# Optimization experiments

Measured on AMD Instinct MI355X. Metric: run time of the kernel, lower is better.

The kernel has to match this reference:

```python
import jax, jax.numpy as jnp
import numpy as np

B, S, HID, NH = 2, 2048, 1024, 16
HD = HID // NH
SCALE = HD ** -0.5


def elu_plus_one(x):
    return jax.nn.elu(x) + 1.0


def setup_inputs() -> dict:
    key = jax.random.key(0)
    ks = jax.random.split(key, 8)
    w_scale = 0.02  # keep logits in a sane range
    return {
        "hidden_states": jax.random.normal(ks[0], (B, S, HID), jnp.float32),
        "wq": jax.random.normal(ks[1], (HID, HID), jnp.float32) * w_scale,
        "wk": jax.random.normal(ks[2], (HID, HID), jnp.float32) * w_scale,
        "wv": jax.random.normal(ks[3], (HID, HID), jnp.float32) * w_scale,
        "wo": jax.random.normal(ks[4], (HID, HID), jnp.float32) * w_scale,
        "beta": jax.random.normal(ks[5], (NH,), jnp.float32),
        "memory": jax.random.normal(ks[6], (NH, HD, HD), jnp.float32),
        "memory_norm": jax.random.uniform(ks[7], (NH, HD), jnp.float32),
    }


def reference(hidden_states, wq, wk, wv, wo, beta, memory, memory_norm):
    b, s, _ = hidden_states.shape
    # nn.Linear(bias=False): x @ W^T; weights stored [out, in]
    def proj(x, w):
        return jnp.einsum("bsh,oh->bso", x, w).reshape(b, s, NH, HD).transpose(0, 2, 1, 3)

    q = proj(hidden_states, wq)  # [B,H,S,D]
    k = proj(hidden_states, wk)
    v = proj(hidden_states, wv)

    # local causal softmax attention (materializes [B,H,S,S] as the original does)
    scores = jnp.einsum("bhsd,bhtd->bhst", q, k) * SCALE
    causal_mask = jnp.triu(jnp.full((s, s), -jnp.inf, dtype=scores.dtype), k=1)
    attn = jax.nn.softmax(scores + causal_mask, axis=-1)
    a_local = jnp.einsum("bhst,bhtd->bhsd", attn, v)

    # compressive memory retrieval: sigma(Q) @ M / (sigma(Q) @ z)
    sigma_q = elu_plus_one(q)
    a_mem_unnorm = jnp.einsum("bhsd,hde->bhse", sigma_q, memory)
    norm = jnp.clip(jnp.einsum("bhsd,hd->bhs", sigma_q, memory_norm), 1e-6, None)
    a_mem = a_mem_unnorm / norm[..., None]

    gate = jax.nn.sigmoid(beta).reshape(1, NH, 1, 1)
    combined = gate * a_mem + (1.0 - gate) * a_local  # [B,H,S,D]
    combined = combined.transpose(0, 2, 1, 3).reshape(b, s, HID)
    return jnp.einsum("bsh,oh->bso", combined, wo)
```

## Files before the change

kernel.cpp:

```cpp
#include <hip/hip_runtime.h>
#include <stdint.h>

#define LOG2E 1.4426950408889634f

typedef __attribute__((ext_vector_type(8))) __bf16 bf16x8;
typedef __attribute__((ext_vector_type(4))) __bf16 bf16x4;
typedef __attribute__((ext_vector_type(4))) float f32x4;

__device__ inline void gll16(const void* g, void* l) {
  __builtin_amdgcn_global_load_lds(
      (const __attribute__((address_space(1))) void*)g,
      (__attribute__((address_space(3))) void*)l, 16, 0, 0);
}

__global__ __launch_bounds__(256) void cvt_all(
    const float* __restrict__ hs, const float* __restrict__ wq,
    const float* __restrict__ wk, const float* __restrict__ wv,
    const float* __restrict__ wo,
    __bf16* __restrict__ hsb, __bf16* __restrict__ wqb, __bf16* __restrict__ wkb,
    __bf16* __restrict__ wvb, __bf16* __restrict__ wob) {
  int bid = blockIdx.x;
  const float* s; __bf16* d; int i;
  if (bid < 4096) { s = hs; d = hsb; i = bid * 256 + threadIdx.x; }
  else {
    int seg = (bid - 4096) >> 10;
    i = ((bid - 4096) & 1023) * 256 + threadIdx.x;
    s = seg == 0 ? wq : seg == 1 ? wk : seg == 2 ? wv : wo;
    d = seg == 0 ? wqb : seg == 1 ? wkb : seg == 2 ? wvb : wob;
  }
  float4 v = ((const float4*)s)[i];
  bf16x4 o;
  o[0] = (__bf16)v.x; o[1] = (__bf16)v.y; o[2] = (__bf16)v.z; o[3] = (__bf16)v.w;
  *(bf16x4*)&d[(size_t)i * 4] = o;
}

#define KSCALE 0.18033688011112042f
__global__ __launch_bounds__(256, 3) void qkv_gemm(
    const __bf16* __restrict__ hsb, const __bf16* __restrict__ wqb,
    const __bf16* __restrict__ wkb, const __bf16* __restrict__ wvb,
    __bf16* __restrict__ qbuf, __bf16* __restrict__ kbuf,
    __bf16* __restrict__ vtb) {
  constexpr int K = 1024;
  __shared__ __align__(16) __bf16 lta[128 * 32];
  __shared__ __align__(16) __bf16 ltb[128 * 32];
  const int bid = blockIdx.x;
  const int z = bid >> 8, r = bid & 255;
  const __bf16 *A, *Bt;
  int m0, n0;
  if (z < 2) {
    A = hsb; Bt = z ? wkb : wqb;
    m0 = (r & 31) * 128; n0 = (r >> 5) * 128;
  } else {
    A = wvb; Bt = hsb;
    m0 = (r & 7) * 128; n0 = (r >> 3) * 128;
  }
  const int tid = threadIdx.x;
  const int w = tid >> 6, l = tid & 63;
  const int lg = l >> 4, lr = l & 15;
  const int wm = (w >> 1) * 64, wn = (w & 1) * 64;
  f32x4 acc[4][4] = {};
  const int srow = w * 16 + (l >> 2);
  const int scol = (l & 3) * 8;
  const __bf16* ga = A + (size_t)(m0 + srow) * K + scol;
  const __bf16* gb = Bt + (size_t)(n0 + srow) * K + scol;
  __bf16* la = &lta[(size_t)w * 16 * 32];
  __bf16* lb = &ltb[(size_t)w * 16 * 32];
  for (int k0 = 0; k0 < K; k0 += 32) {
    __syncthreads();
    gll16(ga + k0, la);
    gll16(ga + 64 * K + k0, la + 64 * 32);
    gll16(gb + k0, lb);
    gll16(gb + 64 * K + k0, lb + 64 * 32);
    __syncthreads();
    bf16x8 af[4], bfr[4];
#pragma unroll
    for (int i = 0; i < 4; ++i) {
      af[i]  = *(const bf16x8*)&lta[(wm + i * 16 + lr) * 32 + lg * 8];
      bfr[i] = *(const bf16x8*)&ltb[(wn + i * 16 + lr) * 32 + lg * 8];
    }
#pragma unroll
    for (int i = 0; i < 4; ++i)
#pragma unroll
      for (int j = 0; j < 4; ++j)
        acc[i][j] = __builtin_amdgcn_mfma_f32_16x16x32_bf16(af[i], bfr[j], acc[i][j], 0, 0, 0);
  }
#pragma unroll
  for (int i = 0; i < 4; ++i)
#pragma unroll
    for (int j = 0; j < 4; ++j)
#pragma unroll
      for (int rr = 0; rr < 4; ++rr) {
        int gm = m0 + wm + i * 16 + lg * 4 + rr;
        int gn = n0 + wn + j * 16 + lr;
        float v = acc[i][j][rr];
        if (z < 2) {
          int bb = gm >> 11, s = gm & 2047, hh = gn >> 6, d = gn & 63;
          __bf16* dst = z ? kbuf : qbuf;
          if (z) v *= KSCALE;
          dst[(((size_t)bb * 16 + hh) * 2048 + s) * 64 + d] = (__bf16)v;
        } else {
          int bb = gn >> 11, s = gn & 2047, hh = gm >> 6, d = gm & 63;
          vtb[(((size_t)bb * 16 + hh) * 64 + d) * 2048 + s] = (__bf16)v;
        }
      }
}

__global__ __launch_bounds__(256, 2) void gemm_out(const __bf16* __restrict__ A,
                                                   const __bf16* __restrict__ Bt,
                                                   float* __restrict__ C,
                                                   int M, int N) {
  constexpr int K = 1024;
  __shared__ __align__(16) __bf16 lta[128 * 32];
  __shared__ __align__(16) __bf16 ltb[64 * 32];
  const int tid = threadIdx.x;
  const int w = tid >> 6, l = tid & 63;
  const int lg = l >> 4, lr = l & 15;
  const int m0 = blockIdx.x * 128, n0 = blockIdx.y * 64;
  const int wm = (w >> 1) * 64, wn = (w & 1) * 32;
  f32x4 acc[4][2] = {};
  const int srow = tid >> 2;
  const int scol = (tid & 3) * 8;
  const __bf16* ga = A + (size_t)(m0 + srow) * K + scol;
  const __bf16* gb = Bt + (size_t)(n0 + srow) * K + scol;
  __bf16* la = &lta[(size_t)w * 512];
  __bf16* lb = &ltb[(size_t)w * 512];
  for (int k0 = 0; k0 < K; k0 += 32) {
    __syncthreads();
    gll16(ga + k0, la);
    gll16(ga + (size_t)64 * K + k0, la + 64 * 32);
    gll16(gb + k0, lb);
    __syncthreads();
    bf16x8 af[4], bfr[2];
#pragma unroll
    for (int i = 0; i < 4; ++i)
      af[i]  = *(const bf16x8*)&lta[(wm + i * 16 + lr) * 32 + lg * 8];
#pragma unroll
    for (int j = 0; j < 2; ++j)
      bfr[j] = *(const bf16x8*)&ltb[(wn + j * 16 + lr) * 32 + lg * 8];
#pragma unroll
    for (int i = 0; i < 4; ++i)
#pragma unroll
      for (int j = 0; j < 2; ++j)
        acc[i][j] = __builtin_amdgcn_mfma_f32_16x16x32_bf16(af[i], bfr[j], acc[i][j], 0, 0, 0);
  }
#pragma unroll
  for (int i = 0; i < 4; ++i)
#pragma unroll
    for (int j = 0; j < 2; ++j)
#pragma unroll
      for (int rr = 0; rr < 4; ++rr) {
        int gm = m0 + wm + i * 16 + lg * 4 + rr;
        int gn = n0 + wn + j * 16 + lr;
        C[(size_t)gm * N + gn] = acc[i][j][rr];
      }
}

#define DEFER_THR 11.5f
#define SWZ(row, col) (((row) << 7) + ((col) ^ (((row) & 7) << 3)))
#define SWZK(row, col) (((row) << 6) + ((col) ^ (((row) & 7) << 3)))

__global__ __launch_bounds__(256, 5) void attn_kernel(
    const __bf16* __restrict__ qb,
    const __bf16* __restrict__ kb,
    const __bf16* __restrict__ vtb,
    const float* __restrict__ memory,
    const float* __restrict__ memnorm,
    const float* __restrict__ beta,
    __bf16* __restrict__ comb)
{
  __shared__ __align__(16) __bf16 kt[128 * 64];
  __shared__ __align__(16) __bf16 vt[64 * 128];

  const int tid = threadIdx.x;
  const int w = tid >> 6, l = tid & 63;
  const int lg = l >> 4, lr = l & 15;
  const int t = 31 - (blockIdx.x >> 5);
  const int bh = blockIdx.x & 31;
  const int hh = bh & 15, b = bh >> 4;
  const int wq0 = t * 64 + w * 16;
  const int ntiles = (t >> 1) + 1;

  const int k_row = tid >> 3;
  const int k_col = ((tid & 7) ^ (k_row & 7)) * 8;
  const __bf16* ksrc = kb + ((size_t)bh * 2048 + k_row) * 64 + k_col;
  const int v_d = tid >> 4;
  const int v_col = ((tid & 15) ^ (v_d & 7)) * 8;
  const __bf16* vsrc = vtb + ((size_t)bh * 64 + v_d) * 2048 + v_col;
  __bf16* kdst = &kt[w * 512];
  __bf16* vdst = &vt[w * 512];

  bf16x8 qf[2];
#pragma unroll
  for (int kk = 0; kk < 2; ++kk)
    qf[kk] = *(const bf16x8*)(qb + ((size_t)bh * 2048 + wq0 + lr) * 64 + kk * 32 + lg * 8);

  float mrun = -1e30f, lsum = 0.f;
  f32x4 apv[4] = {};

  for (int kv = 0; kv < ntiles; ++kv) {
    const int kv0 = kv * 128;
    __syncthreads();
#pragma unroll
    for (int i = 0; i < 4; ++i) {
      gll16(ksrc + (size_t)(kv0 + i * 32) * 64, kdst + i * 2048);
      gll16(vsrc + (size_t)i * 16 * 2048 + kv0, vdst + i * 2048);
    }
    __syncthreads();

    f32x4 sc[8] = {};
#pragma unroll
    for (int kk = 0; kk < 2; ++kk)
#pragma unroll
      for (int nf = 0; nf < 8; ++nf) {
        bf16x8 kf = *(const bf16x8*)&kt[SWZK(nf * 16 + lr, kk * 32 + lg * 8)];
        sc[nf] = __builtin_amdgcn_mfma_f32_16x16x32_bf16(kf, qf[kk], sc[nf], 0, 0, 0);
      }

    const int qrow = wq0 + lr;
    if (kv == ntiles - 1) {
#pragma unroll
      for (int nf = 0; nf < 8; ++nf)
#pragma unroll
        for (int r = 0; r < 4; ++r)
          if (kv0 + nf * 16 + lg * 4 + r > qrow) sc[nf][r] = -1e30f;
    }

    f32x4 m4 = sc[0];
#pragma unroll
    for (int nf = 1; nf < 8; ++nf)
#pragma unroll
      for (int r = 0; r < 4; ++r) m4[r] = fmaxf(m4[r], sc[nf][r]);
    float mx = fmaxf(fmaxf(m4[0], m4[1]), fmaxf(m4[2], m4[3]));
    mx = fmaxf(mx, __shfl_xor(mx, 16, 64));
    mx = fmaxf(mx, __shfl_xor(mx, 32, 64));

    if (!__all(mx - mrun <= DEFER_THR)) {
      float mold = mrun;
      float mn = fmaxf(mold, mx);
      mrun = mn;
      float scl = __builtin_amdgcn_exp2f(mold - mn);
      lsum *= scl;
      float sclq[4];
#pragma unroll
      for (int r = 0; r < 4; ++r) sclq[r] = __shfl(scl, (lg << 2) | r, 16);
#pragma unroll
      for (int nf = 0; nf < 4; ++nf)
#pragma unroll
        for (int r = 0; r < 4; ++r) apv[nf][r] *= sclq[r];
    }

    f32x4 rs4 = {0.f, 0.f, 0.f, 0.f};
#pragma unroll
    for (int nf = 0; nf < 8; ++nf)
#pragma unroll
      for (int r = 0; r < 4; ++r) {
        float pv = __builtin_amdgcn_exp2f(sc[nf][r] - mrun);
        sc[nf][r] = pv;
        rs4[r] += pv;
      }
    float rs = (rs4[0] + rs4[1]) + (rs4[2] + rs4[3]);
    rs += __shfl_xor(rs, 16, 64);
    rs += __shfl_xor(rs, 32, 64);
    lsum += rs;

#pragma unroll
    for (int kk = 0; kk < 4; ++kk) {
      uint32_t a0, a1, b0, b1;
      asm("v_cvt_pk_bf16_f32 %0, %1, %2" : "=v"(a0) : "v"(sc[2 * kk][0]), "v"(sc[2 * kk][1]));
      asm("v_cvt_pk_bf16_f32 %0, %1, %2" : "=v"(a1) : "v"(sc[2 * kk][2]), "v"(sc[2 * kk][3]));
      asm("v_cvt_pk_bf16_f32 %0, %1, %2" : "=v"(b0) : "v"(sc[2 * kk + 1][0]), "v"(sc[2 * kk + 1][1]));
      asm("v_cvt_pk_bf16_f32 %0, %1, %2" : "=v"(b1) : "v"(sc[2 * kk + 1][2]), "v"(sc[2 * kk + 1][3]));
      asm("v_permlane32_swap_b32 %0, %1" : "+v"(a0), "+v"(b0));
      asm("v_permlane32_swap_b32 %0, %1" : "+v"(a1), "+v"(b1));
      asm("v_permlane16_swap_b32 %0, %1" : "+v"(a0), "+v"(b0));
      asm("v_permlane16_swap_b32 %0, %1" : "+v"(a1), "+v"(b1));
      union { uint32_t u[4]; bf16x8 v; } pa;
      pa.u[0] = a0;
      pa.u[1] = a1;
      pa.u[2] = b0;
      pa.u[3] = b1;
#pragma unroll
      for (int nf = 0; nf < 4; ++nf) {
        bf16x8 vf = *(const bf16x8*)&vt[SWZ(nf * 16 + lr, kk * 32 + lg * 8)];
        apv[nf] = __builtin_amdgcn_mfma_f32_16x16x32_bf16(pa.v, vf, apv[nf], 0, 0, 0);
      }
    }
  }

  __syncthreads();
  __bf16* mt = kt;
  for (int i = tid; i < 64 * 64; i += 256) {
    int d = i >> 6, e = i & 63;
    mt[e * 72 + d] = (__bf16)memory[((size_t)hh * 64 + d) * 64 + e];
  }
  for (int i = tid; i < 16 * 64; i += 256) {
    int e = 64 + (i >> 6), d = i & 63;
    mt[e * 72 + d] = (__bf16)memnorm[hh * 64 + d];
  }
  __syncthreads();

  bf16x8 sf[2];
#pragma unroll
  for (int kk = 0; kk < 2; ++kk) {
    bf16x8 q = qf[kk], s;
#pragma unroll
    for (int j = 0; j < 8; ++j) {
      float x = (float)q[j];
      float sg = x > 0.f ? x + 1.f : __builtin_amdgcn_exp2f(x * LOG2E);
      s[j] = (__bf16)sg;
    }
    sf[kk] = s;
  }

  f32x4 am[5] = {};
#pragma unroll
  for (int kk = 0; kk < 2; ++kk)
#pragma unroll
    for (int nf = 0; nf < 5; ++nf) {
      bf16x8 bb = *(const bf16x8*)&mt[(nf * 16 + lr) * 72 + kk * 32 + lg * 8];
      am[nf] = __builtin_amdgcn_mfma_f32_16x16x32_bf16(sf[kk], bb, am[nf], 0, 0, 0);
    }

  const float gate = 1.f / (1.f + __builtin_amdgcn_exp2f(-beta[hh] * LOG2E));
  const float og = 1.f - gate;
  float lsq[4];
#pragma unroll
  for (int r = 0; r < 4; ++r) lsq[r] = __shfl(lsum, (lg << 2) | r, 16);
#pragma unroll
  for (int r = 0; r < 4; ++r) {
    int row = wq0 + lg * 4 + r;
    float linv = __builtin_amdgcn_rcpf(lsq[r]);
    float nrm = fmaxf(am[4][r], 1e-6f);
    float ninv = __builtin_amdgcn_rcpf(nrm);
    size_t base = ((size_t)b * 2048 + row) * 1024 + hh * 64;
#pragma unroll
    for (int nf = 0; nf < 4; ++nf) {
      float al = apv[nf][r] * linv;
      float amv = am[nf][r] * ninv;
      comb[base + nf * 16 + lr] = (__bf16)(gate * amv + og * al);
    }
  }
}

extern "C" void kernel_launch(void* const* d_in, const int* in_sizes, int n_in,
                              void* d_out, int out_size, void* d_ws, size_t ws_size,
                              hipStream_t stream) {
  const float* hs      = (const float*)d_in[0];
  const float* wq      = (const float*)d_in[1];
  const float* wk      = (const float*)d_in[2];
  const float* wv      = (const float*)d_in[3];
  const float* wo      = (const float*)d_in[4];
  const float* beta    = (const float*)d_in[5];
  const float* memory  = (const float*)d_in[6];
  const float* memnorm = (const float*)d_in[7];
  float* out = (float*)d_out;

  char* ws = (char*)d_ws;
  __bf16* hsb  = (__bf16*)(ws);
  __bf16* wqb  = (__bf16*)(ws + ((size_t)8  << 20));
  __bf16* wkb  = (__bf16*)(ws + ((size_t)10 << 20));
  __bf16* wvb  = (__bf16*)(ws + ((size_t)12 << 20));
  __bf16* wob  = (__bf16*)(ws + ((size_t)14 << 20));
  __bf16* qbuf = (__bf16*)(ws + ((size_t)16 << 20));
  __bf16* kbuf = (__bf16*)(ws + ((size_t)24 << 20));
  __bf16* vtb  = (__bf16*)(ws + ((size_t)32 << 20));
  __bf16* comb = (__bf16*)(ws + ((size_t)40 << 20));

  cvt_all<<<8192, 256, 0, stream>>>(hs, wq, wk, wv, wo, hsb, wqb, wkb, wvb, wob);

  qkv_gemm<<<768, 256, 0, stream>>>(hsb, wqb, wkb, wvb, qbuf, kbuf, vtb);

  attn_kernel<<<1024, 256, 0, stream>>>(qbuf, kbuf, vtb, memory, memnorm, beta, comb);

  gemm_out<<<dim3(32, 16), 256, 0, stream>>>(comb, wob, out, 4096, 1024);
}
```

Measured before the change: 104.3 us.

## Split KV range for long causal query tiles and merge partials in separate kernel

The 16 heaviest query-tile rows of the causal attention are each split into two blocks that process halves of the KV range. Each half writes its unnormalized output in bf16 along with its running max and sum. A new merge kernel combines the two halves, computes the memory retrieval and the gate, and writes the combined output. The aim is to even out the load across blocks in the triangular workload. The cost is an extra kernel launch, partial-result traffic through the workspace, and bf16 rounding of the partial outputs. The partials reuse the hsb workspace region, which is safe only because hsb is no longer needed after the QKV GEMM.

```diff
diff --git a/kernel.cpp b/kernel.cpp
--- a/kernel.cpp
+++ b/kernel.cpp
@@ -166,7 +166,9 @@
     const float* __restrict__ memory,
     const float* __restrict__ memnorm,
     const float* __restrict__ beta,
-    __bf16* __restrict__ comb)
+    __bf16* __restrict__ comb,
+    __bf16* __restrict__ pOb,
+    float* __restrict__ pML)
 {
   __shared__ __align__(16) __bf16 kt[128 * 64];
   __shared__ __align__(16) __bf16 vt[64 * 128];
@@ -174,11 +176,17 @@
   const int tid = threadIdx.x;
   const int w = tid >> 6, l = tid & 63;
   const int lg = l >> 4, lr = l & 15;
-  const int t = 31 - (blockIdx.x >> 5);
+  const int idx = blockIdx.x >> 5;
   const int bh = blockIdx.x & 31;
   const int hh = bh & 15, b = bh >> 4;
+  const bool split = idx < 32;
+  const int t = split ? (31 - (idx >> 1)) : (47 - idx);
+  const int half = split ? (idx & 1) : 0;
   const int wq0 = t * 64 + w * 16;
-  const int ntiles = (t >> 1) + 1;
+  const int ntt = (t >> 1) + 1;
+  const int cA = (ntt + 1) >> 1;
+  const int kvb = (split && half) ? cA : 0;
+  const int nloc = split ? (half ? ntt - cA : cA) : ntt;
 
   const int k_row = tid >> 3;
   const int k_col = ((tid & 7) ^ (k_row & 7)) * 8;
@@ -197,8 +205,9 @@
   float mrun = -1e30f, lsum = 0.f;
   f32x4 apv[4] = {};
 
-  for (int kv = 0; kv < ntiles; ++kv) {
-    const int kv0 = kv * 128;
+  for (int kv = 0; kv < nloc; ++kv) {
+    const int kvg = kvb + kv;
+    const int kv0 = kvg * 128;
     __syncthreads();
 #pragma unroll
     for (int i = 0; i < 4; ++i) {
@@ -217,7 +226,7 @@
       }
 
     const int qrow = wq0 + lr;
-    if (kv == ntiles - 1) {
+    if (kvg == ntt - 1) {
 #pragma unroll
       for (int nf = 0; nf < 8; ++nf)
 #pragma unroll
@@ -275,16 +284,27 @@
       asm("v_permlane16_swap_b32 %0, %1" : "+v"(a0), "+v"(b0));
       asm("v_permlane16_swap_b32 %0, %1" : "+v"(a1), "+v"(b1));
       union { uint32_t u[4]; bf16x8 v; } pa;
-      pa.u[0] = a0;
-      pa.u[1] = a1;
-      pa.u[2] = b0;
-      pa.u[3] = b1;
+      pa.u[0] = a0; pa.u[1] = a1; pa.u[2] = b0; pa.u[3] = b1;
 #pragma unroll
       for (int nf = 0; nf < 4; ++nf) {
         bf16x8 vf = *(const bf16x8*)&vt[SWZ(nf * 16 + lr, kk * 32 + lg * 8)];
         apv[nf] = __builtin_amdgcn_mfma_f32_16x16x32_bf16(pa.v, vf, apv[nf], 0, 0, 0);
       }
     }
+  }
+
+  if (split) {
+    const int u = idx * 32 + bh;
+    __bf16* po = pOb + (size_t)u * 4096;
+    float* pml = pML + (size_t)u * 128;
+#pragma unroll
+    for (int nf = 0; nf < 4; ++nf)
+#pragma unroll
+      for (int r = 0; r < 4; ++r)
+        po[(w * 16 + lg * 4 + r) * 64 + nf * 16 + lr] = (__bf16)apv[nf][r];
+    pml[w * 16 + lr] = mrun;
+    pml[64 + w * 16 + lr] = lsum;
+    return;
   }
 
   __syncthreads();
@@ -338,6 +358,92 @@
       float al = apv[nf][r] * linv;
       float amv = am[nf][r] * ninv;
       comb[base + nf * 16 + lr] = (__bf16)(gate * amv + og * al);
+    }
+  }
+}
+
+__global__ __launch_bounds__(256, 2) void attn_merge(
+    const __bf16* __restrict__ qb, const __bf16* __restrict__ pOb,
+    const float* __restrict__ pML, const float* __restrict__ memory,
+    const float* __restrict__ memnorm, const float* __restrict__ beta,
+    __bf16* __restrict__ comb) {
+  __shared__ __align__(16) __bf16 mt[80 * 72];
+  const int tid = threadIdx.x;
+  const int w = tid >> 6, l = tid & 63;
+  const int lg = l >> 4, lr = l & 15;
+  const int tt = blockIdx.x >> 5;
+  const int t = 31 - tt;
+  const int bh = blockIdx.x & 31;
+  const int hh = bh & 15, b = bh >> 4;
+  const int wq0 = t * 64 + w * 16;
+  const int u0 = (tt * 2) * 32 + bh;
+  const int u1 = (tt * 2 + 1) * 32 + bh;
+
+  for (int i = tid; i < 64 * 64; i += 256) {
+    int d = i >> 6, e = i & 63;
+    mt[e * 72 + d] = (__bf16)memory[((size_t)hh * 64 + d) * 64 + e];
+  }
+  for (int i = tid; i < 16 * 64; i += 256) {
+    int e = 64 + (i >> 6), d = i & 63;
+    mt[e * 72 + d] = (__bf16)memnorm[hh * 64 + d];
+  }
+
+  float m1 = pML[(size_t)u0 * 128 + w * 16 + lr];
+  float l1 = pML[(size_t)u0 * 128 + 64 + w * 16 + lr];
+  float m2 = pML[(size_t)u1 * 128 + w * 16 + lr];
+  float l2 = pML[(size_t)u1 * 128 + 64 + w * 16 + lr];
+  float fm = fmaxf(m1, m2);
+  float f1 = __builtin_amdgcn_exp2f(m1 - fm);
+  float f2 = __builtin_amdgcn_exp2f(m2 - fm);
+  float lm = f1 * l1 + f2 * l2;
+
+  bf16x8 qf[2], sf[2];
+#pragma unroll
+  for (int kk = 0; kk < 2; ++kk) {
+    qf[kk] = *(const bf16x8*)(qb + ((size_t)bh * 2048 + wq0 + lr) * 64 + kk * 32 + lg * 8);
+    bf16x8 q = qf[kk], s;
+#pragma unroll
+    for (int j = 0; j < 8; ++j) {
+      float x = (float)q[j];
+      float sg = x > 0.f ? x + 1.f : __builtin_amdgcn_exp2f(x * LOG2E);
+      s[j] = (__bf16)sg;
+    }
+    sf[kk] = s;
+  }
+  __syncthreads();
+
+  f32x4 am[5] = {};
+#pragma unroll
+  for (int kk = 0; kk < 2; ++kk)
+#pragma unroll
+    for (int nf = 0; nf < 5; ++nf) {
+      bf16x8 bb = *(const bf16x8*)&mt[(nf * 16 + lr) * 72 + kk * 32 + lg * 8];
+      am[nf] = __builtin_amdgcn_mfma_f32_16x16x32_bf16(sf[kk], bb, am[nf], 0, 0, 0);
+    }
+
+  const float gate = 1.f / (1.f + __builtin_amdgcn_exp2f(-beta[hh] * LOG2E));
+  const float og = 1.f - gate;
+  float lq[4], f1q[4], f2q[4];
+#pragma unroll
+  for (int r = 0; r < 4; ++r) {
+    lq[r]  = __shfl(lm, (lg << 2) | r, 16);
+    f1q[r] = __shfl(f1, (lg << 2) | r, 16);
+    f2q[r] = __shfl(f2, (lg << 2) | r, 16);
+  }
+  const __bf16* po0 = pOb + (size_t)u0 * 4096;
+  const __bf16* po1 = pOb + (size_t)u1 * 4096;
+#pragma unroll
+  for (int r = 0; r < 4; ++r) {
+    int row = wq0 + lg * 4 + r;
+    float linv = __builtin_amdgcn_rcpf(lq[r]);
+    float nrm = fmaxf(am[4][r], 1e-6f);
+    float ninv = __builtin_amdgcn_rcpf(nrm);
+    size_t base = ((size_t)b * 2048 + row) * 1024 + hh * 64;
+#pragma unroll
+    for (int nf = 0; nf < 4; ++nf) {
+      int off = (w * 16 + lg * 4 + r) * 64 + nf * 16 + lr;
+      float o = f1q[r] * (float)po0[off] + f2q[r] * (float)po1[off];
+      comb[base + nf * 16 + lr] = (__bf16)(gate * am[nf][r] * ninv + og * o * linv);
     }
   }
 }
@@ -365,12 +471,17 @@
   __bf16* kbuf = (__bf16*)(ws + ((size_t)24 << 20));
   __bf16* vtb  = (__bf16*)(ws + ((size_t)32 << 20));
   __bf16* comb = (__bf16*)(ws + ((size_t)40 << 20));
+  __bf16* pOb  = (__bf16*)(ws);
+  float*  pML  = (float*)(ws + ((size_t)8 << 20));
 
   cvt_all<<<8192, 256, 0, stream>>>(hs, wq, wk, wv, wo, hsb, wqb, wkb, wvb, wob);
 
   qkv_gemm<<<768, 256, 0, stream>>>(hsb, wqb, wkb, wvb, qbuf, kbuf, vtb);
 
-  attn_kernel<<<1024, 256, 0, stream>>>(qbuf, kbuf, vtb, memory, memnorm, beta, comb);
+  attn_kernel<<<1536, 256, 0, stream>>>(qbuf, kbuf, vtb, memory, memnorm, beta,
+                                        comb, pOb, pML);
+
+  attn_merge<<<512, 256, 0, stream>>>(qbuf, pOb, pML, memory, memnorm, beta, comb);
 
   gemm_out<<<dim3(32, 16), 256, 0, stream>>>(comb, wob, out, 4096, 1024);
 }
```

After: 116.9 us. +12.0%, slower.
